# Performance work log

Measured on AMD Instinct MI355X. Metric: run time of the kernel, lower is better.

The kernel has to match this reference:

```python
import jax, jax.numpy as jnp
import numpy as np

# SMPL kinematic tree: parent[i] for joint i (root's parent is -1, unused)
PARENTS = [-1, 0, 0, 0, 1, 2, 3, 4, 5, 6, 7, 8, 9, 9, 9, 12, 13, 14, 16, 17, 18, 19, 20, 21]
NUM_JOINTS = 24
NUM_VERTS = 6890
BATCH = 128


def rodrigues(r):
    """r: [K,3] axis-angle -> [K,3,3] rotation (faithful to source, incl. cos(theta*pi)/sin(theta))."""
    eps = 1e-8
    theta = jnp.linalg.norm(r + eps, axis=-1, keepdims=True)  # [K,1]
    r_hat = r / theta                                          # [K,3]
    cos = jnp.cos(theta * jnp.pi)[..., None]                   # [K,1,1]
    sin = jnp.sin(theta)[..., None]                            # [K,1,1]
    rx, ry, rz = r_hat[:, 0], r_hat[:, 1], r_hat[:, 2]
    z = jnp.zeros_like(rx)
    m = jnp.stack([z, -rz, ry, rz, z, -rx, -ry, rx, z], axis=1).reshape(-1, 3, 3)
    eye = jnp.eye(3, dtype=r.dtype)
    dot = r_hat[:, :, None] * r_hat[:, None, :]                # outer product [K,3,3]
    return cos * eye + (1.0 - cos) * dot + sin * m


def setup_inputs() -> dict:
    key = jax.random.key(0)
    k1, k2, k3, k4 = jax.random.split(key, 4)
    V = jax.random.normal(k1, (BATCH, NUM_VERTS, 3), dtype=jnp.float32)
    J = jax.random.normal(k2, (BATCH, NUM_JOINTS, 3), dtype=jnp.float32)
    pose = jax.random.normal(k3, (BATCH, NUM_JOINTS, 3), dtype=jnp.float32)
    W = jax.random.uniform(k4, (BATCH, NUM_VERTS, NUM_JOINTS), dtype=jnp.float32)
    return {"V": V, "J": J, "pose": pose, "W": W}


def reference(V, J, pose, W):
    B = V.shape[0]
    M = NUM_JOINTS
    R = rodrigues(pose.reshape(-1, 3)).reshape(B, M, 3, 3)     # [B,M,3,3]
    # local translations: root uses J[0], others J[i] - J[parent[i]]
    par = np.array(PARENTS[1:])
    t = jnp.concatenate([J[:, :1], J[:, 1:] - J[:, par]], axis=1)  # [B,M,3]
    bottom = jnp.broadcast_to(jnp.array([0.0, 0.0, 0.0, 1.0], dtype=V.dtype), (B, M, 1, 4))
    A = jnp.concatenate([jnp.concatenate([R, t[..., None]], axis=-1), bottom], axis=2)  # [B,M,4,4]
    # forward kinematics along the tree (fixed 24-joint loop; parents always precede children)
    results = [A[:, 0]]
    for i in range(1, M):
        results.append(jnp.matmul(results[PARENTS[i]], A[:, i]))
    G = jnp.stack(results, axis=1)                              # [B,M,4,4]
    # subtract transformed rest-pose joint locations (the 'pack' correction)
    Jh = jnp.concatenate([J, jnp.zeros((B, M, 1), dtype=V.dtype)], axis=-1)  # [B,M,4]
    corr = jnp.einsum('bmij,bmj->bmi', G, Jh)                   # [B,M,4]
    Gc = G - jnp.concatenate([jnp.zeros((B, M, 4, 3), dtype=V.dtype), corr[..., None]], axis=-1)
    # linear blend skinning, without materializing [B,N,M,4,4]
    Tv = jnp.einsum('bnm,bmij->bnij', W, Gc)                    # [B,N,4,4]
    Vh = jnp.concatenate([V, jnp.ones((B, V.shape[1], 1), dtype=V.dtype)], axis=-1)  # [B,N,4]
    out = jnp.einsum('bnij,bnj->bni', Tv, Vh)                   # [B,N,4]
    return out[:, :, :3]
```

## Files before the change

### kernel.cpp

```cpp
#include <hip/hip_runtime.h>
#include <math.h>
#include <string.h>

#define NJ 24
#define NV 6890
#define NB 128

__constant__ int d_anc[NJ][8] = {
  {-1,-1,-1,-1,-1,-1,-1,-1},
  { 0,-1,-1,-1,-1,-1,-1,-1},
  { 0,-1,-1,-1,-1,-1,-1,-1},
  { 0,-1,-1,-1,-1,-1,-1,-1},
  { 1, 0,-1,-1,-1,-1,-1,-1},
  { 2, 0,-1,-1,-1,-1,-1,-1},
  { 3, 0,-1,-1,-1,-1,-1,-1},
  { 4, 1, 0,-1,-1,-1,-1,-1},
  { 5, 2, 0,-1,-1,-1,-1,-1},
  { 6, 3, 0,-1,-1,-1,-1,-1},
  { 7, 4, 1, 0,-1,-1,-1,-1},
  { 8, 5, 2, 0,-1,-1,-1,-1},
  { 9, 6, 3, 0,-1,-1,-1,-1},
  { 9, 6, 3, 0,-1,-1,-1,-1},
  { 9, 6, 3, 0,-1,-1,-1,-1},
  {12, 9, 6, 3, 0,-1,-1,-1},
  {13, 9, 6, 3, 0,-1,-1,-1},
  {14, 9, 6, 3, 0,-1,-1,-1},
  {16,13, 9, 6, 3, 0,-1,-1},
  {17,14, 9, 6, 3, 0,-1,-1},
  {18,16,13, 9, 6, 3, 0,-1},
  {19,17,14, 9, 6, 3, 0,-1},
  {20,18,16,13, 9, 6, 3, 0},
  {21,19,17,14, 9, 6, 3, 0}
};
__constant__ int d_par[NJ] = {-1,0,0,0,1,2,3,4,5,6,7,8,9,9,9,12,13,14,16,17,18,19,20,21};

typedef __attribute__((ext_vector_type(8))) short bf16x8;
typedef __attribute__((ext_vector_type(4))) float f32x4;

__device__ __forceinline__ short f2bf(float f) {
    unsigned int u;
    memcpy(&u, &f, 4);
    u += 0x7fffu + ((u >> 16) & 1u);
    return (short)(u >> 16);
}

#define TLSTRIDE 20

__global__ __launch_bounds__(256) void lbs_fused(const float* __restrict__ V,
                                                 const float* __restrict__ J,
                                                 const float* __restrict__ pose,
                                                 const float* __restrict__ W,
                                                 float* __restrict__ out) {
    const int b   = blockIdx.y;
    const int tid = threadIdx.x;

    __shared__ float A_lds[NJ][12];
    __shared__ float Gc_lds[NJ * 12];
    __shared__ float tl[4 * 64 * TLSTRIDE];

    if (tid < NJ) {
        const int i = tid;
        const float* p = pose + ((size_t)b * NJ + i) * 3;
        float rx = p[0], ry = p[1], rz = p[2];
        float ex = rx + 1e-8f, ey = ry + 1e-8f, ez = rz + 1e-8f;
        float theta = sqrtf(ex * ex + ey * ey + ez * ez);
        float inv = 1.0f / theta;
        float hx = rx * inv, hy = ry * inv, hz = rz * inv;
        float c = cosf(theta * (float)M_PI);
        float s = sinf(theta);
        float oc = 1.0f - c;
        const float* jp = J + ((size_t)b * NJ + i) * 3;
        int par = d_par[i];
        float tx, ty, tz;
        if (par < 0) {
            tx = jp[0]; ty = jp[1]; tz = jp[2];
        } else {
            const float* jq = J + ((size_t)b * NJ + par) * 3;
            tx = jp[0] - jq[0]; ty = jp[1] - jq[1]; tz = jp[2] - jq[2];
        }
        A_lds[i][0]  = c + oc * hx * hx;
        A_lds[i][1]  = oc * hx * hy - s * hz;
        A_lds[i][2]  = oc * hx * hz + s * hy;
        A_lds[i][3]  = tx;
        A_lds[i][4]  = oc * hy * hx + s * hz;
        A_lds[i][5]  = c + oc * hy * hy;
        A_lds[i][6]  = oc * hy * hz - s * hx;
        A_lds[i][7]  = ty;
        A_lds[i][8]  = oc * hz * hx - s * hy;
        A_lds[i][9]  = oc * hz * hy + s * hx;
        A_lds[i][10] = c + oc * hz * hz;
        A_lds[i][11] = tz;
    }
    __syncthreads();

    if (tid < NJ) {
        const int i = tid;
        float M[12];
        #pragma unroll
        for (int j = 0; j < 12; j++) M[j] = A_lds[i][j];

        for (int k = 0; k < 8; k++) {
            int p = d_anc[i][k];
            if (p < 0) break;
            float P[12];
            #pragma unroll
            for (int j = 0; j < 12; j++) P[j] = A_lds[p][j];
            float N[12];
            #pragma unroll
            for (int r = 0; r < 3; r++) {
                float p0 = P[r*4+0], p1 = P[r*4+1], p2 = P[r*4+2], p3 = P[r*4+3];
                N[r*4+0] = p0 * M[0] + p1 * M[4] + p2 * M[8];
                N[r*4+1] = p0 * M[1] + p1 * M[5] + p2 * M[9];
                N[r*4+2] = p0 * M[2] + p1 * M[6] + p2 * M[10];
                N[r*4+3] = p0 * M[3] + p1 * M[7] + p2 * M[11] + p3;
            }
            #pragma unroll
            for (int j = 0; j < 12; j++) M[j] = N[j];
        }

        const float* jp = J + ((size_t)b * NJ + i) * 3;
        float jx = jp[0], jy = jp[1], jz = jp[2];
        #pragma unroll
        for (int r = 0; r < 3; r++) {
            float g0 = M[r*4+0], g1 = M[r*4+1], g2 = M[r*4+2], g3 = M[r*4+3];
            float corr = g0 * jx + g1 * jy + g2 * jz;
            Gc_lds[i*12 + r*4+0] = g0;
            Gc_lds[i*12 + r*4+1] = g1;
            Gc_lds[i*12 + r*4+2] = g2;
            Gc_lds[i*12 + r*4+3] = g3 - corr;
        }
    }
    __syncthreads();

    const int wave  = tid >> 6;
    const int lane  = tid & 63;
    const int vwave = blockIdx.x * 1024 + wave * 256;
    if (vwave >= NV) return;

    float* mytl = &tl[wave * 64 * TLSTRIDE];

    const int n16 = lane & 15;
    const int g   = lane >> 4;

    bf16x8 bfrag;
    #pragma unroll
    for (int j = 0; j < 8; j++) {
        const int k = 8 * g + j;
        const float gval = (k < NJ && n16 < 12) ? Gc_lds[k * 12 + n16] : 0.0f;
        bfrag[j] = f2bf(gval);
    }

    #pragma unroll 1
    for (int grp = 0; grp < 4; grp++) {
        const int gbase = vwave + grp * 64;

        #pragma unroll
        for (int t = 0; t < 4; t++) {
            const int tb = gbase + t * 16;
            const int v  = tb + n16;
            const int vc = v < NV ? v : NV - 1;

            f32x4 lo = {0.f, 0.f, 0.f, 0.f}, hi = {0.f, 0.f, 0.f, 0.f};
            if (g < 3) {
                const float4* wp =
                    (const float4*)(W + ((size_t)b * NV + vc) * 24 + g * 8);
                float4 l4 = wp[0];
                float4 h4 = wp[1];
                lo[0] = l4.x; lo[1] = l4.y; lo[2] = l4.z; lo[3] = l4.w;
                hi[0] = h4.x; hi[1] = h4.y; hi[2] = h4.z; hi[3] = h4.w;
            }
            bf16x8 afrag;
            #pragma unroll
            for (int j = 0; j < 4; j++) afrag[j]     = f2bf(lo[j]);
            #pragma unroll
            for (int j = 0; j < 4; j++) afrag[4 + j] = f2bf(hi[j]);

            f32x4 acc = {0.f, 0.f, 0.f, 0.f};
            acc = __builtin_amdgcn_mfma_f32_16x16x32_bf16(afrag, bfrag, acc, 0, 0, 0);

            #pragma unroll
            for (int r = 0; r < 4; r++) {
                const int lv = t * 16 + 4 * g + r;
                mytl[lv * TLSTRIDE + n16] = acc[r];
            }
        }

        __builtin_amdgcn_wave_barrier();

        const int gv  = gbase + lane;
        const int gvc = gv < NV ? gv : NV - 1;
        const float* row = &mytl[lane * TLSTRIDE];
        f32x4 t0 = *(const f32x4*)(row + 0);
        f32x4 t1 = *(const f32x4*)(row + 4);
        f32x4 t2 = *(const f32x4*)(row + 8);

        const float* vp = V + ((size_t)b * NV + gvc) * 3;
        const float vx = vp[0], vy = vp[1], vz = vp[2];
        if (gv < NV) {
            float* op = out + ((size_t)b * NV + gv) * 3;
            op[0] = t0[0] * vx + t0[1] * vy + t0[2] * vz + t0[3];
            op[1] = t1[0] * vx + t1[1] * vy + t1[2] * vz + t1[3];
            op[2] = t2[0] * vx + t2[1] * vy + t2[2] * vz + t2[3];
        }
        __builtin_amdgcn_wave_barrier();
    }
}

extern "C" void kernel_launch(void* const* d_in, const int* in_sizes, int n_in,
                              void* d_out, int out_size, void* d_ws, size_t ws_size,
                              hipStream_t stream) {
    const float* V    = (const float*)d_in[0];
    const float* J    = (const float*)d_in[1];
    const float* pose = (const float*)d_in[2];
    const float* W    = (const float*)d_in[3];
    float* out = (float*)d_out;

    dim3 grid((NV + 1023) / 1024, NB);
    lbs_fused<<<grid, 256, 0, stream>>>(V, J, pose, W, out);
}
```

Measured before the change: 24.41 us.

## Stage W through LDS with async triple-buffered global_load_lds pipeline

The weight matrix W is now streamed into a triple-buffered LDS ring with async global-to-LDS loads, issued two rounds ahead and overlapped with the joint-transform prologue and the MFMA work. V is prefetched one round ahead in registers. The last block is shifted to end at NV instead of clamping, so some vertices are computed twice but no tail masking is needed. Each round handles 128 vertices at 32 per wave, so half of each wave's lanes sit idle in the epilogue. The kernel also adds a per-round vmcnt(0) wait plus a block barrier, and sets a launch-bounds occupancy hint.

```diff
diff --git a/kernel.cpp b/kernel.cpp
--- a/kernel.cpp
+++ b/kernel.cpp
@@ -5,6 +5,10 @@
 #define NJ 24
 #define NV 6890
 #define NB 128
+#define VPB 1024
+#define VPR 128
+#define NR 8
+#define TLSTRIDE 20
 
 __constant__ int d_anc[NJ][8] = {
   {-1,-1,-1,-1,-1,-1,-1,-1},
@@ -36,6 +40,8 @@
 
 typedef __attribute__((ext_vector_type(8))) short bf16x8;
 typedef __attribute__((ext_vector_type(4))) float f32x4;
+typedef __attribute__((address_space(3))) void lds_vt;
+typedef const __attribute__((address_space(1))) void gm_vt;
 
 __device__ __forceinline__ short f2bf(float f) {
     unsigned int u;
@@ -44,19 +50,45 @@
     return (short)(u >> 16);
 }
 
-#define TLSTRIDE 20
-
-__global__ __launch_bounds__(256) void lbs_fused(const float* __restrict__ V,
-                                                 const float* __restrict__ J,
-                                                 const float* __restrict__ pose,
-                                                 const float* __restrict__ W,
-                                                 float* __restrict__ out) {
-    const int b   = blockIdx.y;
-    const int tid = threadIdx.x;
+__device__ __forceinline__ void stage_round(const float* __restrict__ wsrc,
+                                            float* ldsbuf, int tid) {
+    #pragma unroll
+    for (int i = 0; i < 3; i++) {
+        const int idx = i * 256 + tid;
+        __builtin_amdgcn_global_load_lds((gm_vt*)(wsrc + idx * 4),
+                                         (lds_vt*)(ldsbuf + idx * 4),
+                                         16, 0, 0);
+    }
+}
+
+__global__ __launch_bounds__(256, 3) void lbs_fused(const float* __restrict__ V,
+                                                    const float* __restrict__ J,
+                                                    const float* __restrict__ pose,
+                                                    const float* __restrict__ W,
+                                                    float* __restrict__ out) {
+    const int b    = blockIdx.y;
+    const int tid  = threadIdx.x;
+    const int wave = tid >> 6;
+    const int lane = tid & 63;
+    const int n16  = lane & 15;
+    const int g    = lane >> 4;
+    const int vstart = (blockIdx.x < (NV / VPB)) ? blockIdx.x * VPB : (NV - VPB);
 
     __shared__ float A_lds[NJ][12];
     __shared__ float Gc_lds[NJ * 12];
-    __shared__ float tl[4 * 64 * TLSTRIDE];
+    __shared__ float Wbuf[3][VPR * 24];
+    __shared__ float tl[4 * 32 * TLSTRIDE];
+
+    const float* wbase = W + ((size_t)b * NV + vstart) * 24;
+
+    stage_round(wbase + 0 * VPR * 24, Wbuf[0], tid);
+    stage_round(wbase + 1 * VPR * 24, Wbuf[1], tid);
+
+    float vnx = 0.f, vny = 0.f, vnz = 0.f;
+    if (lane < 32) {
+        const float* vp = V + ((size_t)b * NV + vstart + wave * 32 + lane) * 3;
+        vnx = vp[0]; vny = vp[1]; vnz = vp[2];
+    }
 
     if (tid < NJ) {
         const int i = tid;
@@ -132,15 +164,7 @@
     }
     __syncthreads();
 
-    const int wave  = tid >> 6;
-    const int lane  = tid & 63;
-    const int vwave = blockIdx.x * 1024 + wave * 256;
-    if (vwave >= NV) return;
-
-    float* mytl = &tl[wave * 64 * TLSTRIDE];
-
-    const int n16 = lane & 15;
-    const int g   = lane >> 4;
+    float* mytl = &tl[wave * 32 * TLSTRIDE];
 
     bf16x8 bfrag;
     #pragma unroll
@@ -150,57 +174,53 @@
         bfrag[j] = f2bf(gval);
     }
 
-    #pragma unroll 1
-    for (int grp = 0; grp < 4; grp++) {
-        const int gbase = vwave + grp * 64;
-
+    #pragma unroll
+    for (int r = 0; r < NR; r++) {
+        asm volatile("s_waitcnt vmcnt(0)" ::: "memory");
+        __syncthreads();
+
+        if (r + 2 < NR)
+            stage_round(wbase + (r + 2) * VPR * 24, Wbuf[(r + 2) % 3], tid);
+        const float vcx = vnx, vcy = vny, vcz = vnz;
+        if (lane < 32 && r + 1 < NR) {
+            const float* vp = V + ((size_t)b * NV + vstart + (r + 1) * VPR
+                                   + wave * 32 + lane) * 3;
+            vnx = vp[0]; vny = vp[1]; vnz = vp[2];
+        }
+
+        const float* wb = Wbuf[r % 3];
         #pragma unroll
-        for (int t = 0; t < 4; t++) {
-            const int tb = gbase + t * 16;
-            const int v  = tb + n16;
-            const int vc = v < NV ? v : NV - 1;
-
-            f32x4 lo = {0.f, 0.f, 0.f, 0.f}, hi = {0.f, 0.f, 0.f, 0.f};
+        for (int t = 0; t < 2; t++) {
+            const int lv = wave * 32 + t * 16 + n16;
+            bf16x8 afrag;
             if (g < 3) {
-                const float4* wp =
-                    (const float4*)(W + ((size_t)b * NV + vc) * 24 + g * 8);
-                float4 l4 = wp[0];
-                float4 h4 = wp[1];
-                lo[0] = l4.x; lo[1] = l4.y; lo[2] = l4.z; lo[3] = l4.w;
-                hi[0] = h4.x; hi[1] = h4.y; hi[2] = h4.z; hi[3] = h4.w;
+                f32x4 lo = *(const f32x4*)&wb[lv * 24 + g * 8];
+                f32x4 hi = *(const f32x4*)&wb[lv * 24 + g * 8 + 4];
+                #pragma unroll
+                for (int j = 0; j < 4; j++) { afrag[j] = f2bf(lo[j]); afrag[4+j] = f2bf(hi[j]); }
+            } else {
+                #pragma unroll
+                for (int j = 0; j < 8; j++) afrag[j] = 0;
             }
-            bf16x8 afrag;
-            #pragma unroll
-            for (int j = 0; j < 4; j++) afrag[j]     = f2bf(lo[j]);
-            #pragma unroll
-            for (int j = 0; j < 4; j++) afrag[4 + j] = f2bf(hi[j]);
-
             f32x4 acc = {0.f, 0.f, 0.f, 0.f};
             acc = __builtin_amdgcn_mfma_f32_16x16x32_bf16(afrag, bfrag, acc, 0, 0, 0);
-
-            #pragma unroll
-            for (int r = 0; r < 4; r++) {
-                const int lv = t * 16 + 4 * g + r;
-                mytl[lv * TLSTRIDE + n16] = acc[r];
-            }
+            #pragma unroll
+            for (int rr = 0; rr < 4; rr++)
+                mytl[(t * 16 + 4 * g + rr) * TLSTRIDE + n16] = acc[rr];
         }
 
         __builtin_amdgcn_wave_barrier();
 
-        const int gv  = gbase + lane;
-        const int gvc = gv < NV ? gv : NV - 1;
-        const float* row = &mytl[lane * TLSTRIDE];
-        f32x4 t0 = *(const f32x4*)(row + 0);
-        f32x4 t1 = *(const f32x4*)(row + 4);
-        f32x4 t2 = *(const f32x4*)(row + 8);
-
-        const float* vp = V + ((size_t)b * NV + gvc) * 3;
-        const float vx = vp[0], vy = vp[1], vz = vp[2];
-        if (gv < NV) {
-            float* op = out + ((size_t)b * NV + gv) * 3;
-            op[0] = t0[0] * vx + t0[1] * vy + t0[2] * vz + t0[3];
-            op[1] = t1[0] * vx + t1[1] * vy + t1[2] * vz + t1[3];
-            op[2] = t2[0] * vx + t2[1] * vy + t2[2] * vz + t2[3];
+        if (lane < 32) {
+            const float* row = &mytl[lane * TLSTRIDE];
+            f32x4 t0 = *(const f32x4*)(row + 0);
+            f32x4 t1 = *(const f32x4*)(row + 4);
+            f32x4 t2 = *(const f32x4*)(row + 8);
+            float* op = out + ((size_t)b * NV + vstart + r * VPR
+                               + wave * 32 + lane) * 3;
+            op[0] = t0[0] * vcx + t0[1] * vcy + t0[2] * vcz + t0[3];
+            op[1] = t1[0] * vcx + t1[1] * vcy + t1[2] * vcz + t1[3];
+            op[2] = t2[0] * vcx + t2[1] * vcy + t2[2] * vcz + t2[3];
         }
         __builtin_amdgcn_wave_barrier();
     }
@@ -215,6 +235,6 @@
     const float* W    = (const float*)d_in[3];
     float* out = (float*)d_out;
 
-    dim3 grid((NV + 1023) / 1024, NB);
+    dim3 grid((NV + VPB - 1) / VPB, NB);
     lbs_fused<<<grid, 256, 0, stream>>>(V, J, pose, W, out);
 }
```

Result: slower. 32.35 us (+32.5%).
